# Optimization experiments

Hardware: AMD Instinct MI355X
Metric: run time of the kernel (lower is better)

The kernel has to match this reference:

```python
import jax, jax.numpy as jnp
import numpy as np

N = 100000
E = 1600000
D_IN = 128
D_HID = 128
D_OUT = 128


def _gcn_conv(x, edge_index, W, b):
    # PyG GCNConv: out = D^{-1/2} (A + I) D^{-1/2} (x W) + b
    src, dst = edge_index[0], edge_index[1]
    h = x @ W  # [N, d_out]
    # degree with self-loops, computed on destination nodes
    deg = jax.ops.segment_sum(jnp.ones(src.shape[0], x.dtype), dst, num_segments=N) + 1.0
    dinv = deg ** -0.5  # [N]
    # edge messages: norm_e * h[src]
    norm = dinv[src] * dinv[dst]  # [E]
    msg = h[src] * norm[:, None]  # [E, d_out] -- dominant traffic
    out = jax.ops.segment_sum(msg, dst, num_segments=N)
    # self-loop contribution: norm_ii = dinv[i]^2
    out = out + h * (dinv * dinv)[:, None]
    return out + b


def setup_inputs() -> dict:
    key = jax.random.key(0)
    ks = jax.random.split(key, 8)
    x = jax.random.normal(ks[0], (N, D_IN), dtype=jnp.float32)
    edge_index = jax.random.randint(ks[1], (2, E), 0, N, dtype=jnp.int64)
    def glorot(k, fan_in, fan_out):
        s = (6.0 / (fan_in + fan_out)) ** 0.5
        return jax.random.uniform(k, (fan_in, fan_out), jnp.float32, -s, s)
    return {
        "x": x,
        "edge_index": edge_index,
        "W1": glorot(ks[2], D_IN, D_HID), "b1": jnp.zeros((D_HID,), jnp.float32),
        "W2": glorot(ks[3], D_HID, D_HID), "b2": jnp.zeros((D_HID,), jnp.float32),
        "W3": glorot(ks[4], D_HID, D_OUT), "b3": jnp.zeros((D_OUT,), jnp.float32),
    }


def reference(x, edge_index, W1, b1, W2, b2, W3, b3):
    h = jax.nn.relu(_gcn_conv(x, edge_index, W1, b1))
    h = jax.nn.relu(_gcn_conv(h, edge_index, W2, b2))
    h = jax.nn.relu(_gcn_conv(h, edge_index, W3, b3))
    return h.mean(axis=0)  # [D_OUT]
```

## Files before the change

kernel.cpp:

```cpp
#include <hip/hip_runtime.h>


typedef short bf16x8 __attribute__((ext_vector_type(8)));
typedef float f32x4 __attribute__((ext_vector_type(4)));

__device__ __forceinline__ ushort f2bf(float f) {
  uint u = __builtin_bit_cast(uint, f);
  return (ushort)((u + 0x7fffu + ((u >> 16) & 1u)) >> 16);
}
__device__ __forceinline__ float bflo(uint u) { return __builtin_bit_cast(float, u << 16); }
__device__ __forceinline__ float bfhi(uint u) { return __builtin_bit_cast(float, u & 0xffff0000u); }
__device__ __forceinline__ uint packbf(float x, float y) {
  uint ux = __builtin_bit_cast(uint, x), uy = __builtin_bit_cast(uint, y);
  uint rx = (ux + 0x7fffu + ((ux >> 16) & 1u)) >> 16;
  uint ry = (uy + 0x7fffu + ((uy >> 16) & 1u)) & 0xffff0000u;
  return rx | ry;
}

#define CHUNK 8192

__global__ __launch_bounds__(256) void chist_k(const int* __restrict__ ei,
                                               int* __restrict__ cnt, int e, int nb) {
  __shared__ int h[512];
  int t = threadIdx.x;
  for (int i = t; i < nb; i += 256) h[i] = 0;
  __syncthreads();
  int base = blockIdx.x * CHUNK;
  int lim = min(base + CHUNK, e);
  for (int i = base + t; i < lim; i += 256)
    atomicAdd(&h[ei[e + i] >> 8], 1);
  __syncthreads();
  for (int i = t; i < nb; i += 256) if (h[i]) atomicAdd(&cnt[i], h[i]);
}

__global__ __launch_bounds__(512) void cscan_k(const int* __restrict__ cnt,
                                               int* __restrict__ cbase,
                                               int* __restrict__ ccur,
                                               int* __restrict__ off,
                                               int nb, int n, int e) {
  __shared__ int s[512];
  int t = threadIdx.x;
  int v = (t < nb) ? cnt[t] : 0;
  s[t] = v;
  __syncthreads();
  for (int d = 1; d < 512; d <<= 1) {
    int x = (t >= d) ? s[t - d] : 0;
    __syncthreads();
    s[t] += x;
    __syncthreads();
  }
  int excl = s[t] - v;
  if (t < nb) { cbase[t] = excl; ccur[t] = excl; }
  if (t == 0) { cbase[nb] = e; off[n] = e; }
}

__global__ __launch_bounds__(256) void binscatter_k(const int* __restrict__ ei,
                                                    int* __restrict__ ccur,
                                                    uint* __restrict__ bpak,
                                                    int e, int nb) {
  __shared__ int lhist[512], gbase[512], lcur[512];
  int t = threadIdx.x;
  for (int i = t; i < nb; i += 256) lhist[i] = 0;
  __syncthreads();
  int base = blockIdx.x * CHUNK;
  int lim = min(base + CHUNK, e);
  for (int i = base + t; i < lim; i += 256)
    atomicAdd(&lhist[ei[e + i] >> 8], 1);
  __syncthreads();
  for (int i = t; i < nb; i += 256) {
    int c = lhist[i];
    gbase[i] = c ? atomicAdd(&ccur[i], c) : 0;
    lcur[i] = 0;
  }
  __syncthreads();
  for (int i = base + t; i < lim; i += 256) {
    int d = ei[e + i];
    int s = ei[i];
    int bin = d >> 8;
    int slot = atomicAdd(&lcur[bin], 1);
    bpak[gbase[bin] + slot] = (uint)s | ((uint)(d & 255) << 24);
  }
}

__global__ __launch_bounds__(256) void binsort_k(const uint* __restrict__ bpak,
                                                 const int* __restrict__ cbase,
                                                 float* __restrict__ dinv,
                                                 int* __restrict__ off,
                                                 int* __restrict__ ssrc, int n) {
  __shared__ int hist[256], cur[256], sc[256];
  int b = blockIdx.x, t = threadIdx.x;
  int beg = cbase[b], end = cbase[b + 1];
  hist[t] = 0;
  __syncthreads();
  for (int j = beg + t; j < end; j += 256) atomicAdd(&hist[bpak[j] >> 24], 1);
  __syncthreads();
  int cnt = hist[t];
  sc[t] = cnt;
  __syncthreads();
  for (int d = 1; d < 256; d <<= 1) {
    int x = (t >= d) ? sc[t - d] : 0;
    __syncthreads();
    sc[t] += x;
    __syncthreads();
  }
  int excl = sc[t] - cnt;
  cur[t] = excl;
  int node = b * 256 + t;
  if (node < n) {
    dinv[node] = rsqrtf((float)cnt + 1.0f);
    off[node] = beg + excl;
  }
  __syncthreads();
  for (int j = beg + t; j < end; j += 256) {
    uint pak = bpak[j];
    int pos = atomicAdd(&cur[pak >> 24], 1);
    ssrc[beg + pos] = (int)(pak & 0xFFFFFFu);
  }
}

__global__ __launch_bounds__(256) void wtcast_k(const float* __restrict__ W1,
                                                const float* __restrict__ W2,
                                                const float* __restrict__ W3,
                                                ushort* __restrict__ Wt1,
                                                ushort* __restrict__ Wt2,
                                                ushort* __restrict__ Wt3) {
  int b = blockIdx.x;
  const float* W = (b < 64) ? W1 : ((b < 128) ? W2 : W3);
  ushort* Wt = (b < 64) ? Wt1 : ((b < 128) ? Wt2 : Wt3);
  int idx = (b & 63) * 256 + threadIdx.x;
  int nn = idx >> 7, kk = idx & 127;
  Wt[idx] = f2bf(W[kk * 128 + nn]);
}

template <int EPI>
__global__ __launch_bounds__(256) void gemm_g(
    const void* __restrict__ inv_, const ushort* __restrict__ Wt,
    const float* __restrict__ dinv, const float* __restrict__ bias,
    ushort* __restrict__ outA, int n)
{
  __shared__ ushort sWt[128 * 128];
  const int t = threadIdx.x;

  {
    const uint4* W4 = (const uint4*)Wt;
    uint4* S4 = (uint4*)sWt;
    #pragma unroll
    for (int j = 0; j < 8; ++j) {
      int idx = t + j * 256;
      int row = idx >> 4, slot = idx & 15;
      S4[(row << 4) | (slot ^ (row & 15))] = W4[idx];
    }
  }
  __syncthreads();

  const int wid = t >> 6, lane = t & 63;
  const int rbase = blockIdx.x * 64 + wid * 16;
  if (rbase >= n) return;

  const int l16 = lane & 15, kc = lane >> 4, k0 = kc * 8;
  int arow = rbase + l16;
  bool rok = arow < n;
  int arow_c = rok ? arow : (n - 1);

  bf16x8 afr[4];
  if constexpr (EPI) {
    const ushort* in = (const ushort*)inv_;
    float dv = dinv[arow_c];
    #pragma unroll
    for (int kk = 0; kk < 4; ++kk) {
      uint4 r4 = *(const uint4*)(in + (size_t)arow_c * 128 + kk * 32 + k0);
      float4 bb0 = *(const float4*)(bias + kk * 32 + k0);
      float4 bb1 = *(const float4*)(bias + kk * 32 + k0 + 4);
      uint rr[4] = {r4.x, r4.y, r4.z, r4.w};
      float bb[8] = {bb0.x, bb0.y, bb0.z, bb0.w, bb1.x, bb1.y, bb1.z, bb1.w};
      bf16x8 a;
      #pragma unroll
      for (int q = 0; q < 4; ++q) {
        float lo = fmaxf(fmaf(dv, bflo(rr[q]), bb[2 * q]), 0.f);
        float hi = fmaxf(fmaf(dv, bfhi(rr[q]), bb[2 * q + 1]), 0.f);
        a[2 * q]     = (short)f2bf(lo);
        a[2 * q + 1] = (short)f2bf(hi);
      }
      afr[kk] = rok ? a : (bf16x8)0;
    }
  } else {
    const float4* in4 = (const float4*)inv_;
    #pragma unroll
    for (int kk = 0; kk < 4; ++kk) {
      float4 p0 = in4[(size_t)arow_c * 32 + kk * 8 + kc * 2];
      float4 p1 = in4[(size_t)arow_c * 32 + kk * 8 + kc * 2 + 1];
      float f[8] = {p0.x, p0.y, p0.z, p0.w, p1.x, p1.y, p1.z, p1.w};
      bf16x8 a;
      #pragma unroll
      for (int q = 0; q < 8; ++q) a[q] = (short)f2bf(f[q]);
      afr[kk] = rok ? a : (bf16x8)0;
    }
  }

  f32x4 acc[8];
  #pragma unroll
  for (int nt = 0; nt < 8; ++nt) acc[nt] = (f32x4){0.f, 0.f, 0.f, 0.f};

  #pragma unroll
  for (int kk = 0; kk < 4; ++kk) {
    #pragma unroll
    for (int nt = 0; nt < 8; ++nt) {
      int brow = nt * 16 + l16;
      int bslot = kk * 4 + kc;
      bf16x8 bfr = *(const bf16x8*)(sWt + (((brow << 4) | (bslot ^ (brow & 15))) << 3));
      acc[nt] = __builtin_amdgcn_mfma_f32_16x16x32_bf16(afr[kk], bfr, acc[nt], 0, 0, 0);
    }
  }

  float dvr[4];
  int rr[4];
  #pragma unroll
  for (int j = 0; j < 4; ++j) {
    rr[j] = rbase + kc * 4 + j;
    dvr[j] = (rr[j] < n) ? dinv[rr[j]] : 0.f;
  }
  #pragma unroll
  for (int nt = 0; nt < 8; ++nt) {
    int col = nt * 16 + l16;
    #pragma unroll
    for (int j = 0; j < 4; ++j) {
      if (rr[j] < n)
        outA[(size_t)rr[j] * 128 + col] = f2bf(acc[nt][j] * dvr[j]);
    }
  }
}

__global__ __launch_bounds__(256) void gather_k(const uint* __restrict__ A,
                                                uint* __restrict__ B,
                                                const int* __restrict__ ssrc,
                                                const int* __restrict__ off, int n) {
  int w = (blockIdx.x * 256 + threadIdx.x) >> 6;
  int lane = threadIdx.x & 63;
  if (w >= n) return;
  int beg = off[w], end = off[w + 1];
  uint sv = A[(size_t)w * 64 + lane];
  float ax = bflo(sv), ay = bfhi(sv);
  int j = beg;
  for (; j + 8 <= end; j += 8) {
    uint v0 = A[(size_t)ssrc[j + 0] * 64 + lane];
    uint v1 = A[(size_t)ssrc[j + 1] * 64 + lane];
    uint v2 = A[(size_t)ssrc[j + 2] * 64 + lane];
    uint v3 = A[(size_t)ssrc[j + 3] * 64 + lane];
    uint v4 = A[(size_t)ssrc[j + 4] * 64 + lane];
    uint v5 = A[(size_t)ssrc[j + 5] * 64 + lane];
    uint v6 = A[(size_t)ssrc[j + 6] * 64 + lane];
    uint v7 = A[(size_t)ssrc[j + 7] * 64 + lane];
    ax += ((bflo(v0) + bflo(v1)) + (bflo(v2) + bflo(v3))) +
          ((bflo(v4) + bflo(v5)) + (bflo(v6) + bflo(v7)));
    ay += ((bfhi(v0) + bfhi(v1)) + (bfhi(v2) + bfhi(v3))) +
          ((bfhi(v4) + bfhi(v5)) + (bfhi(v6) + bfhi(v7)));
  }
  for (; j + 4 <= end; j += 4) {
    uint v0 = A[(size_t)ssrc[j + 0] * 64 + lane];
    uint v1 = A[(size_t)ssrc[j + 1] * 64 + lane];
    uint v2 = A[(size_t)ssrc[j + 2] * 64 + lane];
    uint v3 = A[(size_t)ssrc[j + 3] * 64 + lane];
    ax += (bflo(v0) + bflo(v1)) + (bflo(v2) + bflo(v3));
    ay += (bfhi(v0) + bfhi(v1)) + (bfhi(v2) + bfhi(v3));
  }
  for (; j < end; ++j) {
    uint v = A[(size_t)ssrc[j] * 64 + lane];
    ax += bflo(v); ay += bfhi(v);
  }
  B[(size_t)w * 64 + lane] = packbf(ax, ay);
}

__global__ __launch_bounds__(256) void mean1_k(const uint* __restrict__ B,
                                               const float* __restrict__ dinv,
                                               const float* __restrict__ bias,
                                               float* __restrict__ part, int n) {
  __shared__ float s[512];
  int t = threadIdx.x, cg = t & 63, rg = t >> 6;
  float bx = bias[cg * 2], by = bias[cg * 2 + 1];
  float sx = 0.f, sy = 0.f;
  for (int row = blockIdx.x * 4 + rg; row < n; row += 1024) {
    uint v = B[(size_t)row * 64 + cg];
    float dv = dinv[row];
    sx += fmaxf(fmaf(dv, bflo(v), bx), 0.f);
    sy += fmaxf(fmaf(dv, bfhi(v), by), 0.f);
  }
  s[t * 2] = sx; s[t * 2 + 1] = sy;
  __syncthreads();
  if (t < 64) {
    float rx = s[t * 2] + s[(t + 64) * 2] + s[(t + 128) * 2] + s[(t + 192) * 2];
    float ry = s[t * 2 + 1] + s[(t + 64) * 2 + 1] + s[(t + 128) * 2 + 1] + s[(t + 192) * 2 + 1];
    part[blockIdx.x * 128 + cg * 2] = rx;
    part[blockIdx.x * 128 + cg * 2 + 1] = ry;
  }
}

__global__ __launch_bounds__(128) void mean2_k(const float* __restrict__ part,
                                               float* __restrict__ out, float invn) {
  int c = threadIdx.x;
  float s = 0.f;
  for (int b = 0; b < 256; ++b) s += part[b * 128 + c];
  out[c] = s * invn;
}

extern "C" void kernel_launch(void* const* d_in, const int* in_sizes, int n_in,
                              void* d_out, int out_size, void* d_ws, size_t ws_size,
                              hipStream_t stream) {
  const float* x  = (const float*)d_in[0];
  const int*   ei = (const int*)d_in[1];
  const float* W1 = (const float*)d_in[2];
  const float* b1 = (const float*)d_in[3];
  const float* W2 = (const float*)d_in[4];
  const float* b2 = (const float*)d_in[5];
  const float* W3 = (const float*)d_in[6];
  const float* b3 = (const float*)d_in[7];
  float* out = (float*)d_out;

  const int n = in_sizes[0] / 128;
  const int e = in_sizes[1] / 2;
  const int nb = (n + 255) / 256;
  const int nchunk = (e + CHUNK - 1) / CHUNK;

  char* p = (char*)d_ws;
  auto alloc = [&](size_t bytes) {
    char* r = p;
    p += (bytes + 255) & ~(size_t)255;
    return r;
  };
  int*    cnt   = (int*)alloc((size_t)nb * 4);
  int*    cbase = (int*)alloc((size_t)(nb + 1) * 4);
  int*    ccur  = (int*)alloc((size_t)nb * 4);
  int*    off   = (int*)alloc((size_t)(n + 1) * 4);
  float*  dinv  = (float*)alloc((size_t)n * 4);
  uint*   bpak  = (uint*)alloc((size_t)e * 4);
  int*    ssrc  = (int*)alloc((size_t)e * 4);
  ushort* Wt1   = (ushort*)alloc(128 * 128 * 2);
  ushort* Wt2   = (ushort*)alloc(128 * 128 * 2);
  ushort* Wt3   = (ushort*)alloc(128 * 128 * 2);
  ushort* bufA  = (ushort*)alloc((size_t)n * 128 * 2);
  ushort* bufB  = (ushort*)alloc((size_t)n * 128 * 2);
  float*  part  = (float*)alloc(256 * 128 * 4);

  hipMemsetAsync(cnt, 0, (size_t)nb * 4, stream);
  chist_k     <<<nchunk, 256, 0, stream>>>(ei, cnt, e, nb);
  cscan_k     <<<1, 512, 0, stream>>>(cnt, cbase, ccur, off, nb, n, e);
  binscatter_k<<<nchunk, 256, 0, stream>>>(ei, ccur, bpak, e, nb);
  binsort_k   <<<nb, 256, 0, stream>>>(bpak, cbase, dinv, off, ssrc, n);
  wtcast_k    <<<192, 256, 0, stream>>>(W1, W2, W3, Wt1, Wt2, Wt3);

  const int gb = (n + 63) / 64;
  const int ab = (n * 64 + 255) / 256;

  gemm_g<0><<<gb, 256, 0, stream>>>(x, Wt1, dinv, nullptr, bufA, n);
  gather_k <<<ab, 256, 0, stream>>>((const uint*)bufA, (uint*)bufB, ssrc, off, n);
  gemm_g<1><<<gb, 256, 0, stream>>>(bufB, Wt2, dinv, b1, bufA, n);
  gather_k <<<ab, 256, 0, stream>>>((const uint*)bufA, (uint*)bufB, ssrc, off, n);
  gemm_g<1><<<gb, 256, 0, stream>>>(bufB, Wt3, dinv, b2, bufA, n);
  gather_k <<<ab, 256, 0, stream>>>((const uint*)bufA, (uint*)bufB, ssrc, off, n);

  mean1_k<<<256, 256, 0, stream>>>((const uint*)bufB, dinv, b3, part, n);
  mean2_k<<<1, 128, 0, stream>>>(part, out, 1.0f / (float)n);
}
```

Baseline: 433.2 us.

## Store node features in column-slab layout and split gather across eight slabs

Feature matrices become 8 column slabs of 16 bf16 values (32 bytes) per node. The GEMM epilogue, the GEMM input load, the gather and the mean kernel all switch to this layout. Each gather block now handles one slab for 4 nodes, with 8 lanes covering a 32-byte row segment and 8 edge slots processed in parallel, then combined by shuffle reduction. Nontemporal loads and stores are used for indices and outputs. The intent is that each slab's working set (about 3.2 MB) fits better in cache during the random gathers, at the cost of 8x more reads of the index array and smaller 32-byte transactions.

Measured after the change: 1.002 ms. 2.31x slower.

```diff
diff --git a/kernel.cpp b/kernel.cpp
--- a/kernel.cpp
+++ b/kernel.cpp
@@ -140,6 +140,7 @@
 {
   __shared__ ushort sWt[128 * 128];
   const int t = threadIdx.x;
+  const size_t slst = (size_t)n * 16;
 
   {
     const uint4* W4 = (const uint4*)Wt;
@@ -168,7 +169,8 @@
     float dv = dinv[arow_c];
     #pragma unroll
     for (int kk = 0; kk < 4; ++kk) {
-      uint4 r4 = *(const uint4*)(in + (size_t)arow_c * 128 + kk * 32 + k0);
+      int sl = kk * 2 + (kc >> 1);
+      uint4 r4 = *(const uint4*)(in + (size_t)sl * slst + (size_t)arow_c * 16 + (kc & 1) * 8);
       float4 bb0 = *(const float4*)(bias + kk * 32 + k0);
       float4 bb1 = *(const float4*)(bias + kk * 32 + k0 + 4);
       uint rr[4] = {r4.x, r4.y, r4.z, r4.w};
@@ -221,11 +223,11 @@
   }
   #pragma unroll
   for (int nt = 0; nt < 8; ++nt) {
-    int col = nt * 16 + l16;
+    ushort* outs = outA + (size_t)nt * slst + l16;
     #pragma unroll
     for (int j = 0; j < 4; ++j) {
       if (rr[j] < n)
-        outA[(size_t)rr[j] * 128 + col] = f2bf(acc[nt][j] * dvr[j]);
+        outs[(size_t)rr[j] * 16] = f2bf(acc[nt][j] * dvr[j]);
     }
   }
 }
@@ -234,40 +236,36 @@
                                                 uint* __restrict__ B,
                                                 const int* __restrict__ ssrc,
                                                 const int* __restrict__ off, int n) {
-  int w = (blockIdx.x * 256 + threadIdx.x) >> 6;
+  int s = blockIdx.x & 7;
+  int w = (blockIdx.x >> 3) * 4 + (threadIdx.x >> 6);
+  if (w >= n) return;
   int lane = threadIdx.x & 63;
-  if (w >= n) return;
+  int slot = lane >> 3, cu = lane & 7;
+  const uint* As = A + (size_t)s * n * 8;
   int beg = off[w], end = off[w + 1];
-  uint sv = A[(size_t)w * 64 + lane];
-  float ax = bflo(sv), ay = bfhi(sv);
-  int j = beg;
-  for (; j + 8 <= end; j += 8) {
-    uint v0 = A[(size_t)ssrc[j + 0] * 64 + lane];
-    uint v1 = A[(size_t)ssrc[j + 1] * 64 + lane];
-    uint v2 = A[(size_t)ssrc[j + 2] * 64 + lane];
-    uint v3 = A[(size_t)ssrc[j + 3] * 64 + lane];
-    uint v4 = A[(size_t)ssrc[j + 4] * 64 + lane];
-    uint v5 = A[(size_t)ssrc[j + 5] * 64 + lane];
-    uint v6 = A[(size_t)ssrc[j + 6] * 64 + lane];
-    uint v7 = A[(size_t)ssrc[j + 7] * 64 + lane];
-    ax += ((bflo(v0) + bflo(v1)) + (bflo(v2) + bflo(v3))) +
-          ((bflo(v4) + bflo(v5)) + (bflo(v6) + bflo(v7)));
-    ay += ((bfhi(v0) + bfhi(v1)) + (bfhi(v2) + bfhi(v3))) +
-          ((bfhi(v4) + bfhi(v5)) + (bfhi(v6) + bfhi(v7)));
-  }
-  for (; j + 4 <= end; j += 4) {
-    uint v0 = A[(size_t)ssrc[j + 0] * 64 + lane];
-    uint v1 = A[(size_t)ssrc[j + 1] * 64 + lane];
-    uint v2 = A[(size_t)ssrc[j + 2] * 64 + lane];
-    uint v3 = A[(size_t)ssrc[j + 3] * 64 + lane];
-    ax += (bflo(v0) + bflo(v1)) + (bflo(v2) + bflo(v3));
-    ay += (bfhi(v0) + bfhi(v1)) + (bfhi(v2) + bfhi(v3));
-  }
-  for (; j < end; ++j) {
-    uint v = A[(size_t)ssrc[j] * 64 + lane];
-    ax += bflo(v); ay += bfhi(v);
-  }
-  B[(size_t)w * 64 + lane] = packbf(ax, ay);
+  float ax = 0.f, ay = 0.f;
+  int j = beg + slot;
+  for (; j + 8 < end; j += 16) {
+    int s0 = __builtin_nontemporal_load(&ssrc[j]);
+    int s1 = __builtin_nontemporal_load(&ssrc[j + 8]);
+    uint v0 = As[(size_t)s0 * 8 + cu];
+    uint v1 = As[(size_t)s1 * 8 + cu];
+    ax += bflo(v0) + bflo(v1);
+    ay += bfhi(v0) + bfhi(v1);
+  }
+  if (j < end) {
+    int s0 = __builtin_nontemporal_load(&ssrc[j]);
+    uint v0 = As[(size_t)s0 * 8 + cu];
+    ax += bflo(v0); ay += bfhi(v0);
+  }
+  ax += __shfl_xor(ax, 8, 64);  ay += __shfl_xor(ay, 8, 64);
+  ax += __shfl_xor(ax, 16, 64); ay += __shfl_xor(ay, 16, 64);
+  ax += __shfl_xor(ax, 32, 64); ay += __shfl_xor(ay, 32, 64);
+  if (slot == 0) {
+    uint sv = As[(size_t)w * 8 + cu];
+    ax += bflo(sv); ay += bfhi(sv);
+    __builtin_nontemporal_store(packbf(ax, ay), &B[(size_t)s * n * 8 + (size_t)w * 8 + cu]);
+  }
 }
 
 __global__ __launch_bounds__(256) void mean1_k(const uint* __restrict__ B,
@@ -276,10 +274,11 @@
                                                float* __restrict__ part, int n) {
   __shared__ float s[512];
   int t = threadIdx.x, cg = t & 63, rg = t >> 6;
+  const uint* Bs = B + (size_t)(cg >> 3) * n * 8 + (cg & 7);
   float bx = bias[cg * 2], by = bias[cg * 2 + 1];
   float sx = 0.f, sy = 0.f;
   for (int row = blockIdx.x * 4 + rg; row < n; row += 1024) {
-    uint v = B[(size_t)row * 64 + cg];
+    uint v = Bs[(size_t)row * 8];
     float dv = dinv[row];
     sx += fmaxf(fmaf(dv, bflo(v), bx), 0.f);
     sy += fmaxf(fmaf(dv, bfhi(v), by), 0.f);
@@ -348,7 +347,7 @@
   wtcast_k    <<<192, 256, 0, stream>>>(W1, W2, W3, Wt1, Wt2, Wt3);
 
   const int gb = (n + 63) / 64;
-  const int ab = (n * 64 + 255) / 256;
+  const int ab = ((n + 3) / 4) * 8;
 
   gemm_g<0><<<gb, 256, 0, stream>>>(x, Wt1, dinv, nullptr, bufA, n);
   gather_k <<<ab, 256, 0, stream>>>((const uint*)bufA, (uint*)bufB, ssrc, off, n);
```
